# Optimization experiments

Hardware: AMD Instinct MI355X
Metric: run time of the kernel (lower is better)

The kernel has to match this reference:

```python
import jax, jax.numpy as jnp
import numpy as np

N_WIRES = 8
DIM = 2 ** N_WIRES  # 256
NUM_HEADS = 4

def _cnot_ring_perm():
    # Compose CNOT(w, w+1) for w=0..6 then CNOT(7, 0) into one basis permutation.
    # Wire 0 is the most-significant bit of the basis index.
    perm = np.arange(DIM)
    pairs = [(w, w + 1) for w in range(N_WIRES - 1)] + [(N_WIRES - 1, 0)]
    j = np.arange(DIM)
    for c, t in pairs:
        ctrl = (j >> (N_WIRES - 1 - c)) & 1
        M = j ^ (ctrl << (N_WIRES - 1 - t))  # flip target bit where control=1 (involution)
        perm = perm[M]
    return perm

PERM = _cnot_ring_perm()
# SIGNS[i, w] = <i|Z_w|i> = 1 - 2*bit_w(i)
SIGNS = np.array([[1.0 - 2.0 * ((i >> (N_WIRES - 1 - w)) & 1) for w in range(N_WIRES)]
                  for i in range(DIM)], dtype=np.float32)

def setup_inputs() -> dict:
    key = jax.random.key(0)
    k1, k2, k3 = jax.random.split(key, 3)
    x = jax.random.normal(k1, (16, 4096, N_WIRES), jnp.float32)  # rotation angles per token
    theta = jax.random.normal(k2, (N_WIRES,), jnp.float32)       # trainable RX params
    w_combine = jax.random.normal(k3, (N_WIRES, N_WIRES), jnp.float32) / np.float32(np.sqrt(N_WIRES))
    b_combine = jnp.zeros((N_WIRES,), jnp.float32)
    return {"x": x, "theta": theta, "w_combine": w_combine, "b_combine": b_combine}

def _quantum_features(x, theta):
    # RX(x_i) then RX(theta_i) on wire i compose to RX(x_i + theta_i) acting on |0>.
    B, S, E = x.shape
    N = B * S
    phi = (x + theta).reshape(N, E)
    c = jnp.cos(0.5 * phi).astype(jnp.complex64)
    s = (-1j) * jnp.sin(0.5 * phi)          # RX|0> = cos(phi/2)|0> - i sin(phi/2)|1>
    wv = jnp.stack([c, s.astype(jnp.complex64)], axis=-1)  # (N, 8, 2)
    # Build product state via successive Kronecker products (wire 0 = MSB).
    state = jnp.ones((N, 1), jnp.complex64)
    for w in range(E):
        state = (state[:, :, None] * wv[:, w, None, :]).reshape(N, -1)  # (N, 2^(w+1))
    state = state[:, jnp.asarray(PERM)]      # apply the CNOT ring as one permutation
    probs = state.real ** 2 + state.imag ** 2  # (N, 256)
    return (probs @ jnp.asarray(SIGNS)).reshape(B, S, E)  # <Z_w> per token

def reference(x, theta, w_combine, b_combine):
    B, S, E = x.shape
    d_k = E // NUM_HEADS
    q = _quantum_features(x, theta)           # (B, S, 8); k = v = q in the source
    scores = jnp.einsum('bse,bte->bst', q, q) / np.float32(np.sqrt(d_k))
    attn = jax.nn.softmax(scores, axis=-1)    # dropout is identity in eval mode
    out = jnp.einsum('bst,bte->bse', attn, q)
    # Faithful to source: transpose(1,2).contiguous().view(B, S, E)
    out = jnp.swapaxes(out, 1, 2).reshape(B, S, E)
    return out @ w_combine.T + b_combine
```

## Files before the change

kernel.cpp:

```cpp
#include <hip/hip_runtime.h>
#include <math.h>


#define SEQ   4096
#define NB    16
#define SROWS 128
#define TPB   1024
#define NTG   4
#define TC    1024
#define NCH   (SEQ / TC)
#define TILES_PER_TG 8
#define KSTR  12
#define VSTR  1028

typedef _Float16 f16x4  __attribute__((ext_vector_type(4)));
typedef float    f32x16 __attribute__((ext_vector_type(16)));
typedef __fp16   hf2    __attribute__((ext_vector_type(2)));

#if __has_builtin(__builtin_amdgcn_exp2f)
#define EXP2F(x) __builtin_amdgcn_exp2f(x)
#else
#define EXP2F(x) exp2f(x)
#endif

__global__ __launch_bounds__(TPB, 8)
void qattn_kernel(const float* __restrict__ x, const float* __restrict__ theta,
                  const float* __restrict__ wc, const float* __restrict__ bc,
                  float* __restrict__ out)
{
    __shared__ __align__(16) _Float16 kf[TC * KSTR];
    __shared__ __align__(16) _Float16 vt[9 * VSTR];
    float* part = (float*)kf;
    float* attn = (float*)vt;

    const int tid  = threadIdx.x;
    const int lane = tid & 63;
    const int wv   = tid >> 6;
    const int sub  = wv & 3;
    const int tg   = wv >> 2;
    const int l31  = lane & 31;
    const int hp   = lane >> 5;

    const int b  = blockIdx.x >> 5;
    const int S0 = (blockIdx.x & 31) * SROWS;
    const float* xb = x + (size_t)b * SEQ * 8;

    float th[8];
#pragma unroll
    for (int w = 0; w < 8; ++w) th[w] = theta[w];

    vt[8 * VSTR + tid] = (_Float16)1.0f;

    f16x4 qfrag;
    {
        const int s = S0 + sub * 32 + l31;
        const float4 xa  = *(const float4*)(xb + s * 8);
        const float4 xb4 = *(const float4*)(xb + s * 8 + 4);
        float c0 = __cosf(xa.x  + th[0]);
        float c1 = __cosf(xa.y  + th[1]);
        float c2 = __cosf(xa.z  + th[2]);
        float c3 = __cosf(xa.w  + th[3]);
        float c4 = __cosf(xb4.x + th[4]);
        float c5 = __cosf(xb4.y + th[5]);
        float c6 = __cosf(xb4.z + th[6]);
        float c7 = __cosf(xb4.w + th[7]);
        float p1 = c0 * c1, p2 = p1 * c2, p3 = p2 * c3, p4 = p3 * c4;
        float p5 = p4 * c5, p6 = p5 * c6, p7 = p6 * c7;
        float p0 = c1 * c2 * c3 * c4 * c5 * c6 * c7;
        const float sc = 0.70710678118654752f * 1.44269504088896341f;
        if (hp == 0)
            qfrag = (f16x4){(_Float16)(p0*sc), (_Float16)(p1*sc),
                            (_Float16)(p2*sc), (_Float16)(p3*sc)};
        else
            qfrag = (f16x4){(_Float16)(p4*sc), (_Float16)(p5*sc),
                            (_Float16)(p6*sc), (_Float16)(p7*sc)};
    }

    f32x16 o = {0.f,0.f,0.f,0.f,0.f,0.f,0.f,0.f,0.f,0.f,0.f,0.f,0.f,0.f,0.f,0.f};

    const int wr = (l31 < 8) ? l31 : 8;
    const _Float16* kfb = kf + l31 * KSTR + 4 * hp + (tg * TILES_PER_TG) * 32 * KSTR;
    const _Float16* vbb = vt + wr * VSTR + 4 * hp + tg * (TILES_PER_TG * 32);

    float4 pxa = *(const float4*)(xb + tid * 8);
    float4 pxb = *(const float4*)(xb + tid * 8 + 4);

    for (int ch = 0; ch < NCH; ++ch) {
        float c0 = __cosf(pxa.x + th[0]);
        float c1 = __cosf(pxa.y + th[1]);
        float c2 = __cosf(pxa.z + th[2]);
        float c3 = __cosf(pxa.w + th[3]);
        float c4 = __cosf(pxb.x + th[4]);
        float c5 = __cosf(pxb.y + th[5]);
        float c6 = __cosf(pxb.z + th[6]);
        float c7 = __cosf(pxb.w + th[7]);
        float p1 = c0 * c1, p2 = p1 * c2, p3 = p2 * c3, p4 = p3 * c4;
        float p5 = p4 * c5, p6 = p5 * c6, p7 = p6 * c7;
        float p0 = c1 * c2 * c3 * c4 * c5 * c6 * c7;
        _Float16 h0 = (_Float16)p0, h1 = (_Float16)p1, h2 = (_Float16)p2,
                 h3 = (_Float16)p3, h4 = (_Float16)p4, h5 = (_Float16)p5,
                 h6 = (_Float16)p6, h7 = (_Float16)p7;
        __syncthreads();
        {
            _Float16* krow = kf + tid * KSTR;
            *(f16x4*)(krow)     = (f16x4){h0, h1, h2, h3};
            *(f16x4*)(krow + 4) = (f16x4){h4, h5, h6, h7};
            vt[0 * VSTR + tid] = h0;
            vt[1 * VSTR + tid] = h1;
            vt[2 * VSTR + tid] = h2;
            vt[3 * VSTR + tid] = h3;
            vt[4 * VSTR + tid] = h4;
            vt[5 * VSTR + tid] = h5;
            vt[6 * VSTR + tid] = h6;
            vt[7 * VSTR + tid] = h7;
        }
        __syncthreads();
        {
            const int nt = ((ch + 1 < NCH) ? (ch + 1) * TC : ch * TC) + tid;
            pxa = *(const float4*)(xb + nt * 8);
            pxb = *(const float4*)(xb + nt * 8 + 4);
        }
#pragma unroll 4
        for (int i = 0; i < TILES_PER_TG; ++i) {
            f16x4 kfrag = *(const f16x4*)(kfb + i * 32 * KSTR);
            f32x16 cc = __builtin_amdgcn_mfma_f32_32x32x8f16(
                kfrag, qfrag, (f32x16){0.f,0.f,0.f,0.f,0.f,0.f,0.f,0.f,
                                       0.f,0.f,0.f,0.f,0.f,0.f,0.f,0.f}, 0, 0, 0);
#pragma unroll
            for (int u = 0; u < 4; ++u) {
                union { hf2 h[2]; f16x4 v; } pu;
                pu.h[0] = __builtin_amdgcn_cvt_pkrtz(EXP2F(cc[4*u+0]), EXP2F(cc[4*u+1]));
                pu.h[1] = __builtin_amdgcn_cvt_pkrtz(EXP2F(cc[4*u+2]), EXP2F(cc[4*u+3]));
                f16x4 vfrag = *(const f16x4*)(vbb + i * 32 + u * 8);
                o = __builtin_amdgcn_mfma_f32_32x32x8f16(pu.v, vfrag, o, 0, 0, 0);
            }
        }
    }

    __syncthreads();
    if (l31 < 9) {
#pragma unroll
        for (int r = 0; r < 16; ++r) {
            const int sloc = sub * 32 + (r & 3) + 8 * (r >> 2) + 4 * hp;
            part[((tg * SROWS) + sloc) * 9 + l31] = o[r];
        }
    }
    __syncthreads();
    for (int idx = tid; idx < SROWS * 9; idx += TPB) {
        const int rr = idx / 9;
        const int w  = idx - rr * 9;
        float sm = 0.f;
#pragma unroll
        for (int g = 0; g < NTG; ++g) sm += part[((g * SROWS) + rr) * 9 + w];
        attn[rr * 9 + w] = sm;
    }
    __syncthreads();
    if (tid < SROWS * 8) {
        const int rr = tid >> 3;
        const int w  = tid & 7;
        attn[rr * 9 + w] = attn[rr * 9 + w] / attn[rr * 9 + 8];
    }
    __syncthreads();

    if (tid < SROWS) {
        const int e    = tid >> 4;
        const int nloc = tid & 15;
        const int r    = e * 512 + (S0 >> 3) + nloc;
        float y[8];
#pragma unroll
        for (int c = 0; c < 8; ++c) y[c] = attn[(nloc * 8 + c) * 9 + e];
        float oo[8];
#pragma unroll
        for (int k = 0; k < 8; ++k) {
            float a = bc[k];
#pragma unroll
            for (int c = 0; c < 8; ++c) a += y[c] * wc[k * 8 + c];
            oo[k] = a;
        }
        float4* op = (float4*)(out + ((size_t)b * SEQ + r) * 8);
        op[0] = make_float4(oo[0], oo[1], oo[2], oo[3]);
        op[1] = make_float4(oo[4], oo[5], oo[6], oo[7]);
    }
}

extern "C" void kernel_launch(void* const* d_in, const int* in_sizes, int n_in,
                              void* d_out, int out_size, void* d_ws, size_t ws_size,
                              hipStream_t stream)
{
    const float* x  = (const float*)d_in[0];
    const float* th = (const float*)d_in[1];
    const float* wc = (const float*)d_in[2];
    const float* bc = (const float*)d_in[3];
    float* out = (float*)d_out;

    qattn_kernel<<<dim3(NB * (SEQ / SROWS)), dim3(TPB), 0, stream>>>(x, th, wc, bc, out);
}
```

Before: 94.14 us.

## Use 32x32x16 f16 MFMA for PV product with permuted V layout

Swaps the four 32x32x8 MFMAs per tile in the P·V accumulation for two 32x32x16 MFMAs, which are available on gfx950. The V transpose buffer is written with a bit-swapped column index so each lane can load an 8-wide f16 fragment that matches the new K ordering of the exponentiated scores. The V row stride is padded differently to keep 16-byte alignment. This halves the MFMA issue count and V loads per tile, at the cost of a permutation that must exactly match the accumulator register layout.

```diff
diff --git a/kernel.cpp b/kernel.cpp
--- a/kernel.cpp
+++ b/kernel.cpp
@@ -11,9 +11,10 @@
 #define NCH   (SEQ / TC)
 #define TILES_PER_TG 8
 #define KSTR  12
-#define VSTR  1028
+#define VSTR  1032
 
 typedef _Float16 f16x4  __attribute__((ext_vector_type(4)));
+typedef _Float16 f16x8  __attribute__((ext_vector_type(8)));
 typedef float    f32x16 __attribute__((ext_vector_type(16)));
 typedef __fp16   hf2    __attribute__((ext_vector_type(2)));
 
@@ -44,6 +45,8 @@
     const int b  = blockIdx.x >> 5;
     const int S0 = (blockIdx.x & 31) * SROWS;
     const float* xb = x + (size_t)b * SEQ * 8;
+
+    const int pos = (tid & ~12) | ((tid & 4) << 1) | ((tid & 8) >> 1);
 
     float th[8];
 #pragma unroll
@@ -80,7 +83,7 @@
 
     const int wr = (l31 < 8) ? l31 : 8;
     const _Float16* kfb = kf + l31 * KSTR + 4 * hp + (tg * TILES_PER_TG) * 32 * KSTR;
-    const _Float16* vbb = vt + wr * VSTR + 4 * hp + tg * (TILES_PER_TG * 32);
+    const _Float16* vbb = vt + wr * VSTR + 8 * hp + tg * (TILES_PER_TG * 32);
 
     float4 pxa = *(const float4*)(xb + tid * 8);
     float4 pxb = *(const float4*)(xb + tid * 8 + 4);
@@ -105,14 +108,14 @@
             _Float16* krow = kf + tid * KSTR;
             *(f16x4*)(krow)     = (f16x4){h0, h1, h2, h3};
             *(f16x4*)(krow + 4) = (f16x4){h4, h5, h6, h7};
-            vt[0 * VSTR + tid] = h0;
-            vt[1 * VSTR + tid] = h1;
-            vt[2 * VSTR + tid] = h2;
-            vt[3 * VSTR + tid] = h3;
-            vt[4 * VSTR + tid] = h4;
-            vt[5 * VSTR + tid] = h5;
-            vt[6 * VSTR + tid] = h6;
-            vt[7 * VSTR + tid] = h7;
+            vt[0 * VSTR + pos] = h0;
+            vt[1 * VSTR + pos] = h1;
+            vt[2 * VSTR + pos] = h2;
+            vt[3 * VSTR + pos] = h3;
+            vt[4 * VSTR + pos] = h4;
+            vt[5 * VSTR + pos] = h5;
+            vt[6 * VSTR + pos] = h6;
+            vt[7 * VSTR + pos] = h7;
         }
         __syncthreads();
         {
@@ -127,12 +130,14 @@
                 kfrag, qfrag, (f32x16){0.f,0.f,0.f,0.f,0.f,0.f,0.f,0.f,
                                        0.f,0.f,0.f,0.f,0.f,0.f,0.f,0.f}, 0, 0, 0);
 #pragma unroll
-            for (int u = 0; u < 4; ++u) {
-                union { hf2 h[2]; f16x4 v; } pu;
-                pu.h[0] = __builtin_amdgcn_cvt_pkrtz(EXP2F(cc[4*u+0]), EXP2F(cc[4*u+1]));
-                pu.h[1] = __builtin_amdgcn_cvt_pkrtz(EXP2F(cc[4*u+2]), EXP2F(cc[4*u+3]));
-                f16x4 vfrag = *(const f16x4*)(vbb + i * 32 + u * 8);
-                o = __builtin_amdgcn_mfma_f32_32x32x8f16(pu.v, vfrag, o, 0, 0, 0);
+            for (int h = 0; h < 2; ++h) {
+                union { hf2 q[4]; f16x8 v; } pa;
+                pa.q[0] = __builtin_amdgcn_cvt_pkrtz(EXP2F(cc[8*h+0]), EXP2F(cc[8*h+1]));
+                pa.q[1] = __builtin_amdgcn_cvt_pkrtz(EXP2F(cc[8*h+2]), EXP2F(cc[8*h+3]));
+                pa.q[2] = __builtin_amdgcn_cvt_pkrtz(EXP2F(cc[8*h+4]), EXP2F(cc[8*h+5]));
+                pa.q[3] = __builtin_amdgcn_cvt_pkrtz(EXP2F(cc[8*h+6]), EXP2F(cc[8*h+7]));
+                f16x8 vfrag = *(const f16x8*)(vbb + i * 32 + h * 16);
+                o = __builtin_amdgcn_mfma_f32_32x32x16_f16(pa.v, vfrag, o, 0, 0, 0);
             }
         }
     }
```

Result: no change. 92.37 us (-1.9%).
